# Kernel tuning notes

Measured on AMD Instinct MI355X. Metric: run time of the kernel, lower is better.

Reference implementation:

```python
import jax, jax.numpy as jnp
import numpy as np

B, L, H, C, A = 8, 4096, 512, 64, 512
NEG = -1000000000.0

def setup_inputs() -> dict:
    key = jax.random.key(0)
    ks = jax.random.split(key, 6)
    hidden_states = jax.random.normal(ks[0], (B, L, H), dtype=jnp.float32)
    critical_mask = jax.random.randint(ks[1], (B, L, 1), 0, 2).astype(bool)
    count_active_channels = jax.random.randint(ks[2], (B, L, 1), 0, 64).astype(jnp.int32)
    channel_activity = jax.random.normal(ks[3], (B, L, C), dtype=jnp.float32)
    proj_w = jax.random.normal(ks[4], (H, A), dtype=jnp.float32) * 0.02
    proj_b = jnp.zeros((A,), dtype=jnp.float32)
    score_w = jax.random.normal(ks[5], (A, 1), dtype=jnp.float32) * 0.02
    score_b = jnp.zeros((1,), dtype=jnp.float32)
    return {"hidden_states": hidden_states, "critical_mask": critical_mask,
            "count_active_channels": count_active_channels,
            "channel_activity": channel_activity,
            "proj_w": proj_w, "proj_b": proj_b,
            "score_w": score_w, "score_b": score_b}

def reference(hidden_states, critical_mask, count_active_channels, channel_activity,
              proj_w, proj_b, score_w, score_b):
    mask = critical_mask[..., 0].astype(bool)                       # (B,L)
    count_signal = count_active_channels[..., 0].astype(hidden_states.dtype)  # (B,L)
    activity = jnp.maximum(channel_activity.astype(hidden_states.dtype), 0.0)  # (B,L,C)
    # score(tanh(proj(h)))  -> (B,L)
    logits = (jnp.tanh(hidden_states @ proj_w + proj_b) @ score_w + score_b)[..., 0]
    logits = logits + jnp.log1p(jnp.maximum(count_signal, 0.0))
    channel_mask = activity > 0                                      # (B,L,C)
    # (B,C,L) masked logits with log1p activity bias
    channel_logits = logits[:, None, :] + jnp.log1p(jnp.swapaxes(activity, 1, 2))
    channel_logits = jnp.where(jnp.swapaxes(channel_mask, 1, 2), channel_logits, NEG)
    has_channel_any = channel_mask.any(axis=1)                       # (B,C)
    weights = jax.nn.softmax(channel_logits, axis=-1)                # (B,C,L)
    weights = jnp.where(has_channel_any[..., None], weights, 0.0)
    channel_contexts = jnp.einsum('bcl,blh->bch', weights, hidden_states)  # (B,C,H)
    fallback = jnp.broadcast_to(hidden_states[:, -1:, :], channel_contexts.shape)
    channel_contexts = jnp.where(has_channel_any[..., None], channel_contexts, fallback)
    mix = activity / jnp.maximum(activity.sum(axis=2, keepdims=True), 1.0)  # (B,L,C)
    expanded_context = jnp.einsum('blc,bch->blh', mix, channel_contexts)    # (B,L,H)
    max_count = jnp.maximum(count_signal.max(axis=1, keepdims=True), 1.0)
    density_gate = 1.0 + count_signal / max_count                    # (B,L)
    attended = jnp.where(mask[..., None], expanded_context * density_gate[..., None], hidden_states)
    return attended, weights
```

## Files before the change

kernel.cpp:

```cpp
#include <hip/hip_runtime.h>
#include <hip/hip_bf16.h>
#include <math.h>

#define NEGV (-1000000000.0f)
constexpr int Bb = 8, Ll = 4096, Hh = 512, Cc = 64, Aa = 512;

typedef float f32x4 __attribute__((ext_vector_type(4)));
typedef short s16x8 __attribute__((ext_vector_type(8)));

__device__ inline ushort f2bf(float f) {
  union { float f; uint u; } v; v.f = f;
  uint u = v.u;
  return (ushort)((u + 0x7FFFu + ((u >> 16) & 1u)) >> 16);
}

__device__ __forceinline__ void gl16(const void* g, void* l) {
  __builtin_amdgcn_global_load_lds(
      reinterpret_cast<const __attribute__((address_space(1))) unsigned int*>(
          reinterpret_cast<uintptr_t>(g)),
      reinterpret_cast<__attribute__((address_space(3))) unsigned int*>(
          reinterpret_cast<uintptr_t>(l)),
      16, 0, 0);
}

__global__ __launch_bounds__(256) void k_front(
    const float* __restrict__ hid, const int* __restrict__ cnt,
    const float* __restrict__ sb, const float* __restrict__ pw,
    ushort* __restrict__ hidb, ushort* __restrict__ hidbT,
    float* __restrict__ logits, ushort* __restrict__ pwT,
    int* __restrict__ cmax) {
  __shared__ ushort sh[64 * 66];
  const int bid = blockIdx.x;
  const int tid = threadIdx.x;

  if (bid < 4096) {
    const int b = bid >> 9;
    const int rem = bid & 511;
    const int h0 = (rem >> 6) * 64;
    const int l0 = (rem & 63) * 64;
    const int lr = tid >> 5;
    const int hc2 = (tid & 31) * 2;
#pragma unroll
    for (int i = 0; i < 8; ++i) {
      int l = lr * 8 + i;
      float2 f =
          *(const float2*)(hid + ((size_t)(b * Ll + l0 + l)) * Hh + h0 + hc2);
      ushort v0 = f2bf(f.x), v1 = f2bf(f.y);
      *(uint*)(hidb + ((size_t)(b * Ll + l0 + l)) * Hh + h0 + hc2) =
          (uint)v0 | ((uint)v1 << 16);
      sh[l * 66 + hc2] = v0;
      sh[l * 66 + hc2 + 1] = v1;
    }
    __syncthreads();
    const int ht = tid >> 2;
    const int d0 = (tid & 3) * 8;
    uint v[8];
#pragma unroll
    for (int k = 0; k < 8; ++k) {
      int p = d0 + k;
      v[k] = (uint)sh[(2 * p) * 66 + ht] | ((uint)sh[(2 * p + 1) * 66 + ht] << 16);
    }
    ushort* dst = hidbT + ((size_t)(b * Hh + h0 + ht)) * Ll + l0 + 2 * d0;
    *(uint4*)dst = (uint4){v[0], v[1], v[2], v[3]};
    *(uint4*)(dst + 8) = (uint4){v[4], v[5], v[6], v[7]};
  } else if (bid < 4160) {
    const int bx = bid - 4096;
    const int k0 = (bx >> 3) * 64, a0 = (bx & 7) * 64;
#pragma unroll
    for (int i = 0; i < 16; ++i) {
      int e = tid + i * 256;
      int kk = e >> 6, aa = e & 63;
      sh[aa * 65 + kk] = f2bf(pw[(size_t)(k0 + kk) * Aa + a0 + aa]);
    }
    __syncthreads();
#pragma unroll
    for (int i = 0; i < 16; ++i) {
      int e = tid + i * 256;
      int aa = e >> 6, kk = e & 63;
      pwT[(size_t)(a0 + aa) * Hh + k0 + kk] = sh[aa * 65 + kk];
    }
  } else if (bid < 4288) {
    int i = (bid - 4160) * 256 + tid;
    logits[i] = sb[0] + log1pf(fmaxf((float)cnt[i], 0.f));
  } else {
    int* shi = (int*)sh;
    const int b = bid - 4288;
    const int* p = cnt + b * Ll;
    int m = 0;
#pragma unroll
    for (int j = 0; j < 16; ++j) m = max(m, p[tid + j * 256]);
#pragma unroll
    for (int s = 32; s; s >>= 1) m = max(m, __shfl_xor(m, s));
    if ((tid & 63) == 0) shi[tid >> 6] = m;
    __syncthreads();
    if (tid == 0) cmax[b] = max(max(shi[0], shi[1]), max(shi[2], shi[3]));
  }
}

__global__ __launch_bounds__(256) void k0_gemm(
    const ushort* __restrict__ hidb, const ushort* __restrict__ pwT,
    const float* __restrict__ pb, const float* __restrict__ sw,
    float* __restrict__ logits) {
  __shared__ ushort smem[16384];
  const int bm = blockIdx.x, bn = blockIdx.y;
  const int tid = threadIdx.x;
  const int lane = tid & 63;
  const int w = tid >> 6;
  const int wm = w >> 1, wn = w & 1;
  const int lc = lane & 15, lq = lane >> 4;

  const int srow = tid >> 2;
  const int schunk = (tid & 3) * 8;
  const ushort* Ag = hidb + ((size_t)(bm * 128 + srow)) * Hh + schunk;
  const ushort* Bg = pwT + ((size_t)(bn * 128 + srow)) * Hh + schunk;
  const int wrow = 16 * w;

  f32x4 acc[4][4];
#pragma unroll
  for (int mi = 0; mi < 4; ++mi)
#pragma unroll
    for (int ni = 0; ni < 4; ++ni) acc[mi][ni] = (f32x4){0.f, 0.f, 0.f, 0.f};

  const int aoffc = (wm * 64 + lc) * 32 + lq * 8;
  const int boffc = (wn * 64 + lc) * 32 + lq * 8;

#define K0_STAGE(buf, kb)                                   \
  do {                                                      \
    const ushort* ag = Ag + (kb) * 32;                      \
    const ushort* bg = Bg + (kb) * 32;                      \
    ushort* la = smem + (buf) * 4096 + wrow * 32;           \
    ushort* lb = smem + 8192 + (buf) * 4096 + wrow * 32;    \
    gl16(ag, la);                                           \
    gl16(ag + 64 * Hh, la + 64 * 32);                       \
    gl16(bg, lb);                                           \
    gl16(bg + 64 * Hh, lb + 64 * 32);                       \
  } while (0)

  K0_STAGE(0, 0);
  __syncthreads();

  int buf = 0;
  for (int kb = 0; kb < 16; ++kb) {
    if (kb < 15) K0_STAGE(buf ^ 1, kb + 1);
    const ushort* Ab = smem + buf * 4096;
    const ushort* Bt = smem + 8192 + buf * 4096;
    s16x8 af[4], bfr[4];
#pragma unroll
    for (int mi = 0; mi < 4; ++mi)
      af[mi] = *(const s16x8*)(Ab + aoffc + mi * 512);
#pragma unroll
    for (int ni = 0; ni < 4; ++ni)
      bfr[ni] = *(const s16x8*)(Bt + boffc + ni * 512);
#pragma unroll
    for (int mi = 0; mi < 4; ++mi)
#pragma unroll
      for (int ni = 0; ni < 4; ++ni)
        acc[mi][ni] = __builtin_amdgcn_mfma_f32_16x16x32_bf16(
            af[mi], bfr[ni], acc[mi][ni], 0, 0, 0);
    __syncthreads();
    buf ^= 1;
  }
#undef K0_STAGE

  float pbv[4], swv[4];
#pragma unroll
  for (int ni = 0; ni < 4; ++ni) {
    int n = bn * 128 + wn * 64 + ni * 16 + lc;
    pbv[ni] = pb[n];
    swv[ni] = sw[n];
  }
#pragma unroll
  for (int mi = 0; mi < 4; ++mi) {
#pragma unroll
    for (int r = 0; r < 4; ++r) {
      float s = 0.f;
#pragma unroll
      for (int ni = 0; ni < 4; ++ni) {
        float x = acc[mi][ni][r] + pbv[ni];
        float e = __expf(2.f * x);
        float th = 1.f - 2.f / (e + 1.f);
        s = fmaf(th, swv[ni], s);
      }
      s += __shfl_xor(s, 1);
      s += __shfl_xor(s, 2);
      s += __shfl_xor(s, 4);
      s += __shfl_xor(s, 8);
      if (lc == 0) {
        int m = bm * 128 + wm * 64 + mi * 16 + lq * 4 + r;
        atomicAdd(&logits[m], s);
      }
    }
  }
}

__global__ void k2_transpose(const float* __restrict__ act,
                             float* __restrict__ actT,
                             float* __restrict__ dinv) {
  __shared__ float t64[64][65];
  const int b = blockIdx.x >> 6;
  const int l0 = (blockIdx.x & 63) * 64;
  const int tid = threadIdx.x;
#pragma unroll
  for (int i = 0; i < 16; ++i) {
    int e = tid + i * 256;
    int l = e >> 6, c = e & 63;
    float v = act[((size_t)(b * Ll + l0 + l)) * Cc + c];
    t64[l][c] = fmaxf(v, 0.f);
  }
  __syncthreads();
  if (tid < 64) {
    float s = 0.f;
#pragma unroll 8
    for (int c = 0; c < 64; ++c) s += t64[tid][c];
    dinv[b * Ll + l0 + tid] = 1.0f / fmaxf(s, 1.0f);
  }
#pragma unroll
  for (int i = 0; i < 16; ++i) {
    int e = tid + i * 256;
    int c = e >> 6, lq = e & 63;
    actT[((size_t)(b * Cc + c)) * Ll + l0 + lq] = t64[lq][c];
  }
}

__global__ void k3_softmax(const float* __restrict__ actT,
                           const float* __restrict__ logits,
                           float* __restrict__ wout,
                           ushort* __restrict__ wb16,
                           int* __restrict__ hasany) {
  __shared__ float rmax[4], rcnt[4], rsum[4];
  const int bid = blockIdx.x;
  const int b = bid >> 6;
  const int tid = threadIdx.x;
  const float* arow = actT + (size_t)bid * Ll;

  float xs[16];
  float lmax = NEGV, fcnt = 0.f;
#pragma unroll
  for (int i = 0; i < 16; ++i) {
    int l = tid + i * 256;
    float a = arow[l];
    float x;
    if (a > 0.f) {
      x = logits[b * Ll + l] + log1pf(a);
      fcnt += 1.f;
    } else {
      x = NEGV;
    }
    xs[i] = x;
    lmax = fmaxf(lmax, x);
  }
#pragma unroll
  for (int m = 32; m >= 1; m >>= 1) {
    lmax = fmaxf(lmax, __shfl_xor(lmax, m));
    fcnt += __shfl_xor(fcnt, m);
  }
  if ((tid & 63) == 0) { rmax[tid >> 6] = lmax; rcnt[tid >> 6] = fcnt; }
  __syncthreads();
  float m4 = fmaxf(fmaxf(rmax[0], rmax[1]), fmaxf(rmax[2], rmax[3]));
  float call = rcnt[0] + rcnt[1] + rcnt[2] + rcnt[3];

  float lsum = 0.f;
#pragma unroll
  for (int i = 0; i < 16; ++i) {
    float e = expf(xs[i] - m4);
    xs[i] = e;
    lsum += e;
  }
#pragma unroll
  for (int m = 32; m >= 1; m >>= 1) lsum += __shfl_xor(lsum, m);
  if ((tid & 63) == 0) rsum[tid >> 6] = lsum;
  __syncthreads();
  float s = rsum[0] + rsum[1] + rsum[2] + rsum[3];
  int any = call > 0.5f;
  float inv = any ? 1.0f / s : 0.f;
#pragma unroll
  for (int i = 0; i < 16; ++i) {
    float wv = xs[i] * inv;
    wout[(size_t)bid * Ll + tid + i * 256] = wv;
    wb16[(size_t)bid * Ll + tid + i * 256] = f2bf(wv);
  }
  if (tid == 0) hasany[bid] = any;
}

__global__ __launch_bounds__(256) void k5_mfma(
    const ushort* __restrict__ wb16, const ushort* __restrict__ hidbT,
    float* __restrict__ pbuf) {
  const int b = blockIdx.x, nt = blockIdx.y, kz = blockIdx.z;
  const int tid = threadIdx.x;
  const int w = tid >> 6, lane = tid & 63;
  const int lc = lane & 15, lq = lane >> 4;
  const int h0 = nt * 128 + w * 32;

  f32x4 acc[4][2];
#pragma unroll
  for (int mi = 0; mi < 4; ++mi)
#pragma unroll
    for (int ni = 0; ni < 2; ++ni) acc[mi][ni] = (f32x4){0.f, 0.f, 0.f, 0.f};

  const ushort* Abase =
      wb16 + (size_t)b * Cc * Ll + (size_t)lc * Ll + kz * 128 + lq * 8;
  const ushort* Bbase =
      hidbT + ((size_t)(b * Hh + h0 + lc)) * Ll + kz * 128 + lq * 8;

#define K5_LOAD(kb, A, Bv)                                                 \
  do {                                                                     \
    _Pragma("unroll") for (int mi = 0; mi < 4; ++mi) A[mi] =               \
        *(const s16x8*)(Abase + (size_t)mi * 16 * Ll + (kb) * 32);         \
    _Pragma("unroll") for (int ni = 0; ni < 2; ++ni) Bv[ni] =              \
        *(const s16x8*)(Bbase + (size_t)ni * 16 * Ll + (kb) * 32);         \
  } while (0)

#define K5_MFMA(A, Bv)                                                     \
  do {                                                                     \
    _Pragma("unroll") for (int mi = 0; mi < 4; ++mi)                       \
        _Pragma("unroll") for (int ni = 0; ni < 2; ++ni) acc[mi][ni] =     \
            __builtin_amdgcn_mfma_f32_16x16x32_bf16(A[mi], Bv[ni],         \
                                                    acc[mi][ni], 0, 0, 0); \
  } while (0)

  s16x8 aF[4], bF[2], aG[4], bG[2];
  K5_LOAD(0, aF, bF);
  K5_LOAD(1, aG, bG);
  K5_MFMA(aF, bF);
  K5_LOAD(2, aF, bF);
  K5_MFMA(aG, bG);
  K5_LOAD(3, aG, bG);
  K5_MFMA(aF, bF);
  K5_MFMA(aG, bG);
#undef K5_LOAD
#undef K5_MFMA

  const size_t obase = ((size_t)(kz * Bb + b)) * Cc * Hh;
#pragma unroll
  for (int mi = 0; mi < 4; ++mi)
#pragma unroll
    for (int ni = 0; ni < 2; ++ni)
#pragma unroll
      for (int r = 0; r < 4; ++r)
        pbuf[obase + (size_t)(mi * 16 + lq * 4 + r) * Hh + h0 + ni * 16 + lc] =
            acc[mi][ni][r];
}

__global__ void k6_reduce(const float* __restrict__ pbuf,
                          const int* __restrict__ hasany,
                          const float* __restrict__ hid,
                          float* __restrict__ cctx) {
  int idx = blockIdx.x * 256 + threadIdx.x;
  float s = 0.f;
#pragma unroll
  for (int z = 0; z < 32; ++z) s += pbuf[(size_t)z * 262144 + idx];
  int bc = idx >> 9, b = idx >> 15, h = idx & 511;
  cctx[idx] = hasany[bc] ? s : hid[((size_t)(b * Ll + Ll - 1)) * Hh + h];
}

__global__ __launch_bounds__(256) void k7_out(
    const float* __restrict__ hid, const float* __restrict__ act,
    const float* __restrict__ dinv, const float* __restrict__ cctx,
    const int* __restrict__ mask, const int* __restrict__ cnt,
    const int* __restrict__ cmax, float* __restrict__ out) {
  __shared__ float cct[64][128];
  __shared__ float mixs[64][64];
  __shared__ float gateb[64];
  __shared__ int maskb[64];
  const int b = blockIdx.x;
  const int l0 = blockIdx.y * 64;
  const int h0 = blockIdx.z * 128;
  const int tid = threadIdx.x;
  const int w = tid >> 6;

  {
    const float* g = cctx + (size_t)(b * Cc + (tid >> 5)) * Hh + h0 + (tid & 31) * 4;
    float* lb = &cct[0][0] + (2 * w) * 128;
#pragma unroll
    for (int i = 0; i < 8; ++i)
      gl16(g + (size_t)(i * 8) * Hh, lb + i * 8 * 128);
  }
#pragma unroll
  for (int i = 0; i < 4; ++i) {
    int e = tid + i * 256;
    int t = e >> 4, c4 = (e & 15) * 4;
    float4 a4 = *(const float4*)(act + ((size_t)(b * Ll + l0 + t)) * Cc + c4);
    float dv = dinv[b * Ll + l0 + t];
    a4.x = fmaxf(a4.x, 0.f) * dv;
    a4.y = fmaxf(a4.y, 0.f) * dv;
    a4.z = fmaxf(a4.z, 0.f) * dv;
    a4.w = fmaxf(a4.w, 0.f) * dv;
    *(float4*)&mixs[t][c4] = a4;
  }
  if (tid < 64) {
    int l = l0 + tid;
    maskb[tid] = mask[b * Ll + l];
    gateb[tid] = 1.0f + (float)cnt[b * Ll + l] / fmaxf((float)cmax[b], 1.0f);
  }
  __syncthreads();

  const int hcol = (tid & 31) * 4;
  const int tok0 = (tid >> 5) * 8;

  f32x4 acc[8];
#pragma unroll
  for (int t = 0; t < 8; ++t) acc[t] = (f32x4){0.f, 0.f, 0.f, 0.f};

#pragma unroll 4
  for (int c0 = 0; c0 < 64; c0 += 4) {
    f32x4 cv0 = *(const f32x4*)&cct[c0 + 0][hcol];
    f32x4 cv1 = *(const f32x4*)&cct[c0 + 1][hcol];
    f32x4 cv2 = *(const f32x4*)&cct[c0 + 2][hcol];
    f32x4 cv3 = *(const f32x4*)&cct[c0 + 3][hcol];
#pragma unroll
    for (int t = 0; t < 8; ++t) {
      f32x4 mv = *(const f32x4*)&mixs[tok0 + t][c0];
      f32x4 a = acc[t];
      a = cv0 * mv.x + a;
      a = cv1 * mv.y + a;
      a = cv2 * mv.z + a;
      a = cv3 * mv.w + a;
      acc[t] = a;
    }
  }

#pragma unroll
  for (int t = 0; t < 8; ++t) {
    int tok = tok0 + t;
    size_t off = ((size_t)(b * Ll + l0 + tok)) * Hh + h0 + hcol;
    f32x4 o;
    if (maskb[tok]) {
      o = acc[t] * gateb[tok];
    } else {
      o = *(const f32x4*)(hid + off);
    }
    *(f32x4*)(out + off) = o;
  }
}

extern "C" void kernel_launch(void* const* d_in, const int* in_sizes, int n_in,
                              void* d_out, int out_size, void* d_ws,
                              size_t ws_size, hipStream_t stream) {
  const float* hid = (const float*)d_in[0];
  const int* mask = (const int*)d_in[1];
  const int* cnt = (const int*)d_in[2];
  const float* act = (const float*)d_in[3];
  const float* pw = (const float*)d_in[4];
  const float* pb = (const float*)d_in[5];
  const float* sw = (const float*)d_in[6];
  const float* sb = (const float*)d_in[7];

  float* out_att = (float*)d_out;
  float* out_w = out_att + (size_t)Bb * Ll * Hh;

  float* ws = (float*)d_ws;
  float* cctx = ws;
  int* cmaxi = (int*)(ws + 262144);
  float* logits = ws + 262152;
  float* actT = ws + 294920;
  float* dinv = ws + 2392072;
  int* hasany = (int*)(ws + 2424840);
  ushort* pwT = (ushort*)(ws + 2425352);
  ushort* wb16 = (ushort*)(ws + 2556424);
  float* pbuf = ws + 3605000;

  ushort* hidb = (ushort*)out_att;
  ushort* hidbT = (ushort*)(out_att + 8388608);

  k_front<<<4296, 256, 0, stream>>>(hid, cnt, sb, pw, hidb, hidbT, logits,
                                    pwT, cmaxi);
  k0_gemm<<<dim3(256, 4), 256, 0, stream>>>(hidb, pwT, pb, sw, logits);
  k2_transpose<<<512, 256, 0, stream>>>(act, actT, dinv);
  k3_softmax<<<512, 256, 0, stream>>>(actT, logits, out_w, wb16, hasany);
  k5_mfma<<<dim3(8, 4, 32), 256, 0, stream>>>(wb16, hidbT, pbuf);
  k6_reduce<<<1024, 256, 0, stream>>>(pbuf, hasany, hid, cctx);
  k7_out<<<dim3(8, 64, 4), 256, 0, stream>>>(hid, act, dinv, cctx, mask, cnt,
                                             cmaxi, out_att);
}
```

Before: 260.0 us.

## Fold transpose into front kernel and replace split-K reduce with atomics

Moves the activity transpose and dinv computation into the front kernel as extra blocks, and adds blocks there that zero the channel-context buffer. The split-K context GEMM now covers twice the K range per block (16 splits instead of 32) and accumulates straight into cctx with atomicAdd, which removes the partial buffer and the separate reduce kernel. The fallback to the last hidden row for empty channels is applied in the output kernel's shared-memory tile. The aim is fewer launches and less partial-sum traffic, at the cost of atomic contention and non-deterministic summation order.

```diff
diff --git a/kernel.cpp b/kernel.cpp
--- a/kernel.cpp
+++ b/kernel.cpp
@@ -26,10 +26,13 @@
 __global__ __launch_bounds__(256) void k_front(
     const float* __restrict__ hid, const int* __restrict__ cnt,
     const float* __restrict__ sb, const float* __restrict__ pw,
-    ushort* __restrict__ hidb, ushort* __restrict__ hidbT,
-    float* __restrict__ logits, ushort* __restrict__ pwT,
-    int* __restrict__ cmax) {
-  __shared__ ushort sh[64 * 66];
+    const float* __restrict__ act, ushort* __restrict__ hidb,
+    ushort* __restrict__ hidbT, float* __restrict__ logits,
+    ushort* __restrict__ pwT, int* __restrict__ cmax,
+    float* __restrict__ actT, float* __restrict__ dinv,
+    float* __restrict__ cctx) {
+  __shared__ float shf[64 * 65];
+  ushort* sh = (ushort*)shf;
   const int bid = blockIdx.x;
   const int tid = threadIdx.x;
 
@@ -82,8 +85,8 @@
   } else if (bid < 4288) {
     int i = (bid - 4160) * 256 + tid;
     logits[i] = sb[0] + log1pf(fmaxf((float)cnt[i], 0.f));
-  } else {
-    int* shi = (int*)sh;
+  } else if (bid < 4296) {
+    int* shi = (int*)shf;
     const int b = bid - 4288;
     const int* p = cnt + b * Ll;
     int m = 0;
@@ -94,6 +97,38 @@
     if ((tid & 63) == 0) shi[tid >> 6] = m;
     __syncthreads();
     if (tid == 0) cmax[b] = max(max(shi[0], shi[1]), max(shi[2], shi[3]));
+  } else if (bid < 4808) {
+    const int bx = bid - 4296;
+    const int b = bx >> 6;
+    const int l0 = (bx & 63) * 64;
+#pragma unroll
+    for (int i = 0; i < 16; ++i) {
+      int e = tid + i * 256;
+      int l = e >> 6, c = e & 63;
+      float v = act[((size_t)(b * Ll + l0 + l)) * Cc + c];
+      shf[l * 65 + c] = fmaxf(v, 0.f);
+    }
+    __syncthreads();
+    if (tid < 64) {
+      float s = 0.f;
+#pragma unroll 8
+      for (int c = 0; c < 64; ++c) s += shf[tid * 65 + c];
+      dinv[b * Ll + l0 + tid] = 1.0f / fmaxf(s, 1.0f);
+    }
+#pragma unroll
+    for (int i = 0; i < 16; ++i) {
+      int e = tid + i * 256;
+      int c = e >> 6, lq = e & 63;
+      actT[((size_t)(b * Cc + c)) * Ll + l0 + lq] = shf[lq * 65 + c];
+    }
+  } else {
+    const int bz = bid - 4808;
+    float* p = cctx + ((size_t)(bz * 256 + tid)) * 16;
+    f32x4 z = (f32x4){0.f, 0.f, 0.f, 0.f};
+    *(f32x4*)(p + 0) = z;
+    *(f32x4*)(p + 4) = z;
+    *(f32x4*)(p + 8) = z;
+    *(f32x4*)(p + 12) = z;
   }
 }
 
@@ -193,35 +228,6 @@
   }
 }
 
-__global__ void k2_transpose(const float* __restrict__ act,
-                             float* __restrict__ actT,
-                             float* __restrict__ dinv) {
-  __shared__ float t64[64][65];
-  const int b = blockIdx.x >> 6;
-  const int l0 = (blockIdx.x & 63) * 64;
-  const int tid = threadIdx.x;
-#pragma unroll
-  for (int i = 0; i < 16; ++i) {
-    int e = tid + i * 256;
-    int l = e >> 6, c = e & 63;
-    float v = act[((size_t)(b * Ll + l0 + l)) * Cc + c];
-    t64[l][c] = fmaxf(v, 0.f);
-  }
-  __syncthreads();
-  if (tid < 64) {
-    float s = 0.f;
-#pragma unroll 8
-    for (int c = 0; c < 64; ++c) s += t64[tid][c];
-    dinv[b * Ll + l0 + tid] = 1.0f / fmaxf(s, 1.0f);
-  }
-#pragma unroll
-  for (int i = 0; i < 16; ++i) {
-    int e = tid + i * 256;
-    int c = e >> 6, lq = e & 63;
-    actT[((size_t)(b * Cc + c)) * Ll + l0 + lq] = t64[lq][c];
-  }
-}
-
 __global__ void k3_softmax(const float* __restrict__ actT,
                            const float* __restrict__ logits,
                            float* __restrict__ wout,
@@ -284,7 +290,7 @@
 
 __global__ __launch_bounds__(256) void k5_mfma(
     const ushort* __restrict__ wb16, const ushort* __restrict__ hidbT,
-    float* __restrict__ pbuf) {
+    float* __restrict__ cctx) {
   const int b = blockIdx.x, nt = blockIdx.y, kz = blockIdx.z;
   const int tid = threadIdx.x;
   const int w = tid >> 6, lane = tid & 63;
@@ -298,9 +304,9 @@
     for (int ni = 0; ni < 2; ++ni) acc[mi][ni] = (f32x4){0.f, 0.f, 0.f, 0.f};
 
   const ushort* Abase =
-      wb16 + (size_t)b * Cc * Ll + (size_t)lc * Ll + kz * 128 + lq * 8;
+      wb16 + (size_t)b * Cc * Ll + (size_t)lc * Ll + kz * 256 + lq * 8;
   const ushort* Bbase =
-      hidbT + ((size_t)(b * Hh + h0 + lc)) * Ll + kz * 128 + lq * 8;
+      hidbT + ((size_t)(b * Hh + h0 + lc)) * Ll + kz * 256 + lq * 8;
 
 #define K5_LOAD(kb, A, Bv)                                                 \
   do {                                                                     \
@@ -326,38 +332,35 @@
   K5_MFMA(aG, bG);
   K5_LOAD(3, aG, bG);
   K5_MFMA(aF, bF);
+  K5_LOAD(4, aF, bF);
+  K5_MFMA(aG, bG);
+  K5_LOAD(5, aG, bG);
+  K5_MFMA(aF, bF);
+  K5_LOAD(6, aF, bF);
+  K5_MFMA(aG, bG);
+  K5_LOAD(7, aG, bG);
+  K5_MFMA(aF, bF);
   K5_MFMA(aG, bG);
 #undef K5_LOAD
 #undef K5_MFMA
 
-  const size_t obase = ((size_t)(kz * Bb + b)) * Cc * Hh;
 #pragma unroll
   for (int mi = 0; mi < 4; ++mi)
 #pragma unroll
     for (int ni = 0; ni < 2; ++ni)
 #pragma unroll
       for (int r = 0; r < 4; ++r)
-        pbuf[obase + (size_t)(mi * 16 + lq * 4 + r) * Hh + h0 + ni * 16 + lc] =
-            acc[mi][ni][r];
-}
-
-__global__ void k6_reduce(const float* __restrict__ pbuf,
-                          const int* __restrict__ hasany,
-                          const float* __restrict__ hid,
-                          float* __restrict__ cctx) {
-  int idx = blockIdx.x * 256 + threadIdx.x;
-  float s = 0.f;
-#pragma unroll
-  for (int z = 0; z < 32; ++z) s += pbuf[(size_t)z * 262144 + idx];
-  int bc = idx >> 9, b = idx >> 15, h = idx & 511;
-  cctx[idx] = hasany[bc] ? s : hid[((size_t)(b * Ll + Ll - 1)) * Hh + h];
+        atomicAdd(&cctx[((size_t)(b * Cc + mi * 16 + lq * 4 + r)) * Hh + h0 +
+                        ni * 16 + lc],
+                  acc[mi][ni][r]);
 }
 
 __global__ __launch_bounds__(256) void k7_out(
     const float* __restrict__ hid, const float* __restrict__ act,
     const float* __restrict__ dinv, const float* __restrict__ cctx,
-    const int* __restrict__ mask, const int* __restrict__ cnt,
-    const int* __restrict__ cmax, float* __restrict__ out) {
+    const int* __restrict__ hasany, const int* __restrict__ mask,
+    const int* __restrict__ cnt, const int* __restrict__ cmax,
+    float* __restrict__ out) {
   __shared__ float cct[64][128];
   __shared__ float mixs[64][64];
   __shared__ float gateb[64];
@@ -391,6 +394,16 @@
     int l = l0 + tid;
     maskb[tid] = mask[b * Ll + l];
     gateb[tid] = 1.0f + (float)cnt[b * Ll + l] / fmaxf((float)cmax[b], 1.0f);
+  }
+  __syncthreads();
+
+  {
+    int c = tid >> 2, hq = (tid & 3) * 32;
+    if (!hasany[b * Cc + c]) {
+      const float* hl = hid + ((size_t)(b * Ll + Ll - 1)) * Hh + h0 + hq;
+#pragma unroll 8
+      for (int j = 0; j < 32; ++j) cct[c][hq + j] = hl[j];
+    }
   }
   __syncthreads();
 
@@ -457,18 +470,15 @@
   int* hasany = (int*)(ws + 2424840);
   ushort* pwT = (ushort*)(ws + 2425352);
   ushort* wb16 = (ushort*)(ws + 2556424);
-  float* pbuf = ws + 3605000;
 
   ushort* hidb = (ushort*)out_att;
   ushort* hidbT = (ushort*)(out_att + 8388608);
 
-  k_front<<<4296, 256, 0, stream>>>(hid, cnt, sb, pw, hidb, hidbT, logits,
-                                    pwT, cmaxi);
+  k_front<<<4872, 256, 0, stream>>>(hid, cnt, sb, pw, act, hidb, hidbT,
+                                    logits, pwT, cmaxi, actT, dinv, cctx);
   k0_gemm<<<dim3(256, 4), 256, 0, stream>>>(hidb, pwT, pb, sw, logits);
-  k2_transpose<<<512, 256, 0, stream>>>(act, actT, dinv);
   k3_softmax<<<512, 256, 0, stream>>>(actT, logits, out_w, wb16, hasany);
-  k5_mfma<<<dim3(8, 4, 32), 256, 0, stream>>>(wb16, hidbT, pbuf);
-  k6_reduce<<<1024, 256, 0, stream>>>(pbuf, hasany, hid, cctx);
-  k7_out<<<dim3(8, 64, 4), 256, 0, stream>>>(hid, act, dinv, cctx, mask, cnt,
-                                             cmaxi, out_att);
-}
+  k5_mfma<<<dim3(8, 4, 16), 256, 0, stream>>>(wb16, hidbT, cctx);
+  k7_out<<<dim3(8, 64, 4), 256, 0, stream>>>(hid, act, dinv, cctx, hasany,
+                                             mask, cnt, cmaxi, out_att);
+}
```

Measured after the change: 256.8 us. Within noise of the previous version (-1.2%).
